# Performance work log

Hardware: AMD Instinct MI355X
Metric: run time of the kernel (lower is better)

## Reference

```python
import jax, jax.numpy as jnp
import numpy as np

V_A, V_HP = 256, 256
H_A, H_HP = 2048, 4096
DEPTH = 12


def lstm_cell(x, h, c, W_ih, W_hh, b_ih, b_hh):
    # PyTorch LSTM cell: gate order i, f, g, o along the 4H axis.
    gates = x @ W_ih.T + h @ W_hh.T + (b_ih + b_hh)
    i, f, g, o = jnp.split(gates, 4, axis=-1)
    c_new = jax.nn.sigmoid(f) * c + jax.nn.sigmoid(i) * jnp.tanh(g)
    h_new = jax.nn.sigmoid(o) * jnp.tanh(c_new)
    return h_new, c_new


def setup_inputs() -> dict:
    key = jax.random.key(0)
    ks = jax.random.split(key, 16)
    s = jnp.float32(0.02)
    f32 = jnp.float32
    return {
        "x_thought_vec_arch": jax.random.normal(ks[0], (1, 1, H_A), f32),
        "x_thought_vec_arch_hp": jax.random.normal(ks[1], (1, 1, H_HP), f32),
        # arch LSTM (input V_A, hidden H_A)
        "W_ih_a": jax.random.normal(ks[2], (4 * H_A, V_A), f32) * s,
        "W_hh_a": jax.random.normal(ks[3], (4 * H_A, H_A), f32) * s,
        "b_ih_a": jax.random.normal(ks[4], (4 * H_A,), f32) * s,
        "b_hh_a": jax.random.normal(ks[5], (4 * H_A,), f32) * s,
        # arch_out Linear (H_A -> V_A)
        "W_out_a": jax.random.normal(ks[6], (V_A, H_A), f32) * s,
        "b_out_a": jax.random.normal(ks[7], (V_A,), f32) * s,
        # hp_summarizer Linear (H_HP -> H_HP//2)
        "W_sum": jax.random.normal(ks[8], (H_HP // 2, H_HP), f32) * s,
        "b_sum": jax.random.normal(ks[9], (H_HP // 2,), f32) * s,
        # arch_hp LSTM (input V_A + V_HP, hidden H_HP)
        "W_ih_hp": jax.random.normal(ks[10], (4 * H_HP, V_A + V_HP), f32) * s,
        "W_hh_hp": jax.random.normal(ks[11], (4 * H_HP, H_HP), f32) * s,
        "b_ih_hp": jax.random.normal(ks[12], (4 * H_HP,), f32) * s,
        "b_hh_hp": jax.random.normal(ks[13], (4 * H_HP,), f32) * s,
        # arch_hp_out Linear (H_HP -> V_HP)
        "W_out_hp": jax.random.normal(ks[14], (V_HP, H_HP), f32) * s,
        "b_out_hp": jax.random.normal(ks[15], (V_HP,), f32) * s,
    }


def reference(x_thought_vec_arch, x_thought_vec_arch_hp,
              W_ih_a, W_hh_a, b_ih_a, b_hh_a, W_out_a, b_out_a,
              W_sum, b_sum, W_ih_hp, W_hh_hp, b_ih_hp, b_hh_hp,
              W_out_hp, b_out_hp):
    h_a, h_hp = x_thought_vec_arch, x_thought_vec_arch_hp  # thought vecs used as hidden states
    c_a = jnp.zeros_like(h_a)
    c_hp = jnp.zeros_like(h_hp)
    a = jnp.full((1, 1, V_A), 1.0 / V_A, jnp.float32)       # SOS soft one-hot
    a_hp = jnp.full((1, 1, V_HP), 1.0 / V_HP, jnp.float32)

    def step(carry, _):
        a, a_hp, h_a, c_a, h_hp, c_hp = carry
        # forward_arch: seq_len=1 so LSTM output == new hidden
        h_a, c_a = lstm_cell(a, h_a, c_a, W_ih_a, W_hh_a, b_ih_a, b_hh_a)
        a = jax.nn.softmax(h_a @ W_out_a.T + b_out_a, axis=-1)
        # forward_arch_hp (keeps the original's swapped hx=(c_hp, prev_h_hp)):
        h_sum = jax.nn.relu(h_hp @ W_sum.T + b_sum)
        prev_h_hp = jnp.concatenate([h_a, h_sum], axis=-1)   # used as CELL state
        inp = jnp.concatenate([a, a_hp], axis=-1)
        h_hp, c_hp = lstm_cell(inp, c_hp, prev_h_hp, W_ih_hp, W_hh_hp, b_ih_hp, b_hh_hp)
        a_hp = jax.nn.softmax(h_hp @ W_out_hp.T + b_out_hp, axis=-1)
        return (a, a_hp, h_a, c_a, h_hp, c_hp), (a, a_hp)

    _, (ys_a, ys_hp) = jax.lax.scan(step, (a, a_hp, h_a, c_a, h_hp, c_hp), None, length=DEPTH)
    # torch.cat(list_of_(1,1,V), dim=1) -> (1, DEPTH, V)
    arch = ys_a.reshape(DEPTH, V_A)[None]
    arch_hp = ys_hp.reshape(DEPTH, V_HP)[None]
    return arch, arch_hp
```

## Files before the change

kernel.cpp:

```cpp
#include <hip/hip_runtime.h>
#include <hip/hip_fp16.h>

#define H_A   2048
#define H_HP  4096
#define V_A   256
#define V_HP  256
#define DEPTH 12

struct Half8 { __half2 a, b, c, d; };

__device__ __forceinline__ float fsig_(float x) { return 1.0f / (1.0f + __expf(-x)); }
__device__ __forceinline__ float ftanh_(float x) {
    return 1.0f - 2.0f / (__expf(2.0f * x) + 1.0f);
}

__device__ __forceinline__ float dot8h_(Half8 w, float4 x0, float4 x1) {
    float2 wa = __half22float2(w.a), wb = __half22float2(w.b);
    float2 wc = __half22float2(w.c), wd = __half22float2(w.d);
    return wa.x * x0.x + wa.y * x0.y + wb.x * x0.z + wb.y * x0.w +
           wc.x * x1.x + wc.y * x1.y + wd.x * x1.z + wd.y * x1.w;
}

__device__ __forceinline__ Half8 cvt8_(float4 a, float4 b) {
    Half8 h;
    h.a = __floats2half2_rn(a.x, a.y);
    h.b = __floats2half2_rn(a.z, a.w);
    h.c = __floats2half2_rn(b.x, b.y);
    h.d = __floats2half2_rn(b.z, b.w);
    return h;
}

__device__ __forceinline__ float waveReduceSum(float v) {
#pragma unroll
    for (int off = 32; off > 0; off >>= 1) v += __shfl_xor(v, off, 64);
    return v;
}

__global__ void k_init(const float* __restrict__ x_a, const float* __restrict__ x_hp,
                       float* __restrict__ h_a, float* __restrict__ c_a0,
                       float* __restrict__ h_hp, float* __restrict__ c_hp,
                       float* __restrict__ a_vec, float* __restrict__ logits_hp)
{
    int i = blockIdx.x * 256 + threadIdx.x;
    if (i < H_A)  { h_a[i] = x_a[i];  c_a0[i] = 0.0f; }
    if (i < H_HP) { h_hp[i] = x_hp[i]; c_hp[i] = 0.0f; }
    if (i < V_A)  { a_vec[i] = 1.0f / 256.0f; logits_hp[i] = 0.0f; }
}

__global__ __launch_bounds__(256) void k_f2h_batched(
    const float* __restrict__ W_ih_a,  __half* __restrict__ hW_ih_a,
    const float* __restrict__ W_hh_a,  __half* __restrict__ hW_hh_a,
    const float* __restrict__ W_sum,   __half* __restrict__ hW_sum,
    const float* __restrict__ W_ih_hp, __half* __restrict__ hW_ih_hp,
    const float* __restrict__ W_out_a, __half* __restrict__ hW_out_a,
    const float* __restrict__ W_out_hp,__half* __restrict__ hW_out_hp)
{
    int i = blockIdx.x * 256 + threadIdx.x;
    const float* src; __half* dst; int base;
    if      (i < 262144)  { src = W_ih_a;   dst = hW_ih_a;   base = 0; }
    else if (i < 2359296) { src = W_hh_a;   dst = hW_hh_a;   base = 262144; }
    else if (i < 3407872) { src = W_sum;    dst = hW_sum;    base = 2359296; }
    else if (i < 4456448) { src = W_ih_hp;  dst = hW_ih_hp;  base = 3407872; }
    else if (i < 4521984) { src = W_out_a;  dst = hW_out_a;  base = 4456448; }
    else if (i < 4653056) { src = W_out_hp; dst = hW_out_hp; base = 4521984; }
    else return;
    int j = i - base;
    float4 a = ((const float4*)src)[2 * j];
    float4 b = ((const float4*)src)[2 * j + 1];
    ((Half8*)dst)[j] = cvt8_(a, b);
}

__global__ __launch_bounds__(256) void kA_fused_gemv(
    const __half* __restrict__ hW_ih_a, const __half* __restrict__ hW_hh_a,
    const float* __restrict__ b_ih_a, const float* __restrict__ b_hh_a,
    const __half* __restrict__ hW_sum,  const float* __restrict__ b_sum,
    __half* __restrict__ hW_hh_hp, const float* __restrict__ W_hh_hp_f32,
    const float* __restrict__ b_ih_hp, const float* __restrict__ b_hh_hp,
    const float* __restrict__ a_vec,  const float* __restrict__ h_a,
    const float* __restrict__ h_hp,   const float* __restrict__ c_hp,
    float* __restrict__ gates_a, float* __restrict__ h_sum_o,
    float* __restrict__ gacc_hp, int step0)
{
    const int lane = threadIdx.x & 63;
    const int wave = (blockIdx.x << 2) | (threadIdx.x >> 6);

    if (wave < 8192) {
        const int r = wave;
        const __half2* wp = (const __half2*)(hW_ih_a + (size_t)r * V_A);
        __half2 w0h = wp[2 * lane], w1h = wp[2 * lane + 1];
        float4 x = ((const float4*)a_vec)[lane];
        float2 w0 = __half22float2(w0h), w1 = __half22float2(w1h);
        float acc = w0.x * x.x + w0.y * x.y + w1.x * x.z + w1.y * x.w;
        const Half8* wh = (const Half8*)(hW_hh_a + (size_t)r * H_A);
        const float4* xh = (const float4*)h_a;
#pragma unroll
        for (int it = 0; it < 4; ++it) {
            int idx = it * 64 + lane;
            acc += dot8h_(wh[idx], xh[2 * idx], xh[2 * idx + 1]);
        }
        acc = waveReduceSum(acc);
        if (lane == 0) gates_a[r] = acc + b_ih_a[r] + b_hh_a[r];
    } else if (wave < 10240) {
        const int r = wave - 8192;
        const Half8* ww = (const Half8*)(hW_sum + (size_t)r * H_HP);
        const float4* xx = (const float4*)h_hp;
        float acc = 0.0f;
#pragma unroll
        for (int it = 0; it < 8; ++it) {
            int idx = it * 64 + lane;
            acc += dot8h_(ww[idx], xx[2 * idx], xx[2 * idx + 1]);
        }
        acc = waveReduceSum(acc);
        if (lane == 0) h_sum_o[r] = fmaxf(acc + b_sum[r], 0.0f);
    } else {
        const int r = wave - 10240;
        if (step0) {
            const float4* src = (const float4*)(W_hh_hp_f32 + (size_t)r * H_HP);
            Half8* dst = (Half8*)(hW_hh_hp + (size_t)r * H_HP);
#pragma unroll
            for (int it = 0; it < 8; ++it) {
                int idx = it * 64 + lane;
                dst[idx] = cvt8_(src[2 * idx], src[2 * idx + 1]);
            }
            if (lane == 0) gacc_hp[r] = b_ih_hp[r] + b_hh_hp[r];
        } else {
            const Half8* ww = (const Half8*)(hW_hh_hp + (size_t)r * H_HP);
            const float4* xx = (const float4*)c_hp;
            float acc = 0.0f;
#pragma unroll
            for (int it = 0; it < 8; ++it) {
                int idx = it * 64 + lane;
                acc += dot8h_(ww[idx], xx[2 * idx], xx[2 * idx + 1]);
            }
            acc = waveReduceSum(acc);
            if (lane == 0) gacc_hp[r] = acc + b_ih_hp[r] + b_hh_hp[r];
        }
    }
}

__global__ __launch_bounds__(256) void kB_arch(
    const float* __restrict__ gates_a, const float* __restrict__ c_in,
    float* __restrict__ c_out, float* __restrict__ h_a_g,
    const __half* __restrict__ hW_out_a, const float* __restrict__ b_out_a,
    float* __restrict__ logits_a)
{
    __shared__ float h_s[H_A];
    const int t = threadIdx.x;
#pragma unroll
    for (int k = 0; k < 8; ++k) {
        int e = t + k * 256;
        float gi = gates_a[e];
        float gf = gates_a[H_A + e];
        float gg = gates_a[2 * H_A + e];
        float go = gates_a[3 * H_A + e];
        float c_new = fsig_(gf) * c_in[e] + fsig_(gi) * ftanh_(gg);
        float h = fsig_(go) * ftanh_(c_new);
        h_s[e] = h;
        if (blockIdx.x == 0) { c_out[e] = c_new; h_a_g[e] = h; }
    }
    __syncthreads();
    const int lane = t & 63;
    const int r = (blockIdx.x << 2) | (t >> 6);
    const Half8* w8 = (const Half8*)(hW_out_a + (size_t)r * H_A);
    const float4* h4 = (const float4*)h_s;
    float acc = 0.0f;
#pragma unroll
    for (int it = 0; it < 4; ++it) {
        int idx = it * 64 + lane;
        acc += dot8h_(w8[idx], h4[2 * idx], h4[2 * idx + 1]);
    }
    acc = waveReduceSum(acc);
    if (lane == 0) logits_a[r] = acc + b_out_a[r];
}

__global__ __launch_bounds__(256) void kC_softmax_ih(
    const float* __restrict__ logits_a, const float* __restrict__ logits_hp,
    const __half* __restrict__ hW_ih_hp, float* __restrict__ gacc_hp,
    float* __restrict__ a_vec_g, float* __restrict__ out_a,
    float* __restrict__ out_hp)
{
    __shared__ float p_all[512];
    __shared__ float red[8];
    const int t = threadIdx.x, lane = t & 63, wv = t >> 6;
    float la = logits_a[t], lh = logits_hp[t];
    float ma = la, mh = lh;
#pragma unroll
    for (int off = 32; off > 0; off >>= 1) {
        ma = fmaxf(ma, __shfl_xor(ma, off, 64));
        mh = fmaxf(mh, __shfl_xor(mh, off, 64));
    }
    if (lane == 0) { red[wv] = ma; red[4 + wv] = mh; }
    __syncthreads();
    ma = fmaxf(fmaxf(red[0], red[1]), fmaxf(red[2], red[3]));
    mh = fmaxf(fmaxf(red[4], red[5]), fmaxf(red[6], red[7]));
    __syncthreads();
    float ea = __expf(la - ma), eh = __expf(lh - mh);
    float sa = waveReduceSum(ea), sh = waveReduceSum(eh);
    if (lane == 0) { red[wv] = sa; red[4 + wv] = sh; }
    __syncthreads();
    sa = red[0] + red[1] + red[2] + red[3];
    sh = red[4] + red[5] + red[6] + red[7];
    float pa = ea / sa, ph = eh / sh;
    p_all[t] = pa;
    p_all[256 + t] = ph;
    if (blockIdx.x == 0) {
        a_vec_g[t] = pa;
        out_a[t] = pa;
        out_hp[t] = ph;
    }
    __syncthreads();
    const float4* x4 = (const float4*)p_all;
    float4 xa = x4[2 * lane], xb = x4[2 * lane + 1];
    const int gw = (blockIdx.x << 2) | wv;
#pragma unroll
    for (int rr = 0; rr < 4; ++rr) {
        int r = (gw << 2) | rr;
        Half8 w = ((const Half8*)(hW_ih_hp + (size_t)r * (V_A + V_HP)))[lane];
        float acc = dot8h_(w, xa, xb);
        acc = waveReduceSum(acc);
        if (lane == 0) gacc_hp[r] += acc;
    }
}

__global__ __launch_bounds__(256) void kD_hp(
    const float* __restrict__ gacc_hp, const float* __restrict__ h_a,
    const float* __restrict__ h_sum, float* __restrict__ c_hp_g,
    float* __restrict__ h_hp_g,
    const __half* __restrict__ hW_out_hp, const float* __restrict__ b_out_hp,
    float* __restrict__ logits_hp)
{
    __shared__ float h_s[H_HP];
    const int t = threadIdx.x;
#pragma unroll
    for (int k = 0; k < 16; ++k) {
        int e = t + k * 256;
        float gi = gacc_hp[e];
        float gf = gacc_hp[H_HP + e];
        float gg = gacc_hp[2 * H_HP + e];
        float go = gacc_hp[3 * H_HP + e];
        float prev = (e < H_A) ? h_a[e] : h_sum[e - H_A];
        float c = fsig_(gf) * prev + fsig_(gi) * ftanh_(gg);
        float h = fsig_(go) * ftanh_(c);
        h_s[e] = h;
        if (blockIdx.x == 0) { c_hp_g[e] = c; h_hp_g[e] = h; }
    }
    __syncthreads();
    const int lane = t & 63;
    const int r = (blockIdx.x << 2) | (t >> 6);
    const Half8* w8 = (const Half8*)(hW_out_hp + (size_t)r * H_HP);
    const float4* x4 = (const float4*)h_s;
    float acc = 0.0f;
#pragma unroll
    for (int it = 0; it < 8; ++it) {
        int idx = it * 64 + lane;
        acc += dot8h_(w8[idx], x4[2 * idx], x4[2 * idx + 1]);
    }
    acc = waveReduceSum(acc);
    if (lane == 0) logits_hp[r] = acc + b_out_hp[r];
}

__global__ __launch_bounds__(256) void k_softmax_tail(
    const float* __restrict__ logits_hp, float* __restrict__ outp)
{
    __shared__ float red[4];
    const int t = threadIdx.x, lane = t & 63, wv = t >> 6;
    float v = logits_hp[t];
    float m = v;
#pragma unroll
    for (int off = 32; off > 0; off >>= 1) m = fmaxf(m, __shfl_xor(m, off, 64));
    if (lane == 0) red[wv] = m;
    __syncthreads();
    m = fmaxf(fmaxf(red[0], red[1]), fmaxf(red[2], red[3]));
    __syncthreads();
    float e = __expf(v - m);
    float s = waveReduceSum(e);
    if (lane == 0) red[wv] = s;
    __syncthreads();
    s = red[0] + red[1] + red[2] + red[3];
    outp[t] = e / s;
}


extern "C" void kernel_launch(void* const* d_in, const int* in_sizes, int n_in,
                              void* d_out, int out_size, void* d_ws, size_t ws_size,
                              hipStream_t stream)
{
    const float* x_a      = (const float*)d_in[0];
    const float* x_hp     = (const float*)d_in[1];
    const float* W_ih_a   = (const float*)d_in[2];
    const float* W_hh_a   = (const float*)d_in[3];
    const float* b_ih_a   = (const float*)d_in[4];
    const float* b_hh_a   = (const float*)d_in[5];
    const float* W_out_a  = (const float*)d_in[6];
    const float* b_out_a  = (const float*)d_in[7];
    const float* W_sum    = (const float*)d_in[8];
    const float* b_sum    = (const float*)d_in[9];
    const float* W_ih_hp  = (const float*)d_in[10];
    const float* W_hh_hp  = (const float*)d_in[11];
    const float* b_ih_hp  = (const float*)d_in[12];
    const float* b_hh_hp  = (const float*)d_in[13];
    const float* W_out_hp = (const float*)d_in[14];
    const float* b_out_hp = (const float*)d_in[15];

    float* out = (float*)d_out;

    __half* hW_ih_a   = (__half*)d_ws;
    __half* hW_hh_a   = hW_ih_a   + 2097152;
    __half* hW_sum    = hW_hh_a   + 16777216;
    __half* hW_ih_hp  = hW_sum    + 8388608;
    __half* hW_hh_hp  = hW_ih_hp  + 8388608;
    __half* hW_out_a  = hW_hh_hp  + 67108864;
    __half* hW_out_hp = hW_out_a  + 524288;
    float* ws = (float*)(hW_out_hp + 1048576);

    float* gates_a   = ws;
    float* h_sum     = ws + 8192;
    float* gacc_hp   = ws + 10240;
    float* h_a       = ws + 26624;
    float* c_a0      = ws + 28672;
    float* c_a1      = ws + 30720;
    float* h_hp      = ws + 32768;
    float* c_hp      = ws + 36864;
    float* logits_a  = ws + 40960;
    float* logits_hp = ws + 41216;
    float* a_vec     = ws + 41472;
    float* dummy     = ws + 41728;
    float* c_a[2]    = { c_a0, c_a1 };

    k_init<<<16, 256, 0, stream>>>(x_a, x_hp, h_a, c_a0, h_hp, c_hp, a_vec, logits_hp);

    k_f2h_batched<<<18176, 256, 0, stream>>>(
        W_ih_a, hW_ih_a, W_hh_a, hW_hh_a, W_sum, hW_sum,
        W_ih_hp, hW_ih_hp, W_out_a, hW_out_a, W_out_hp, hW_out_hp);

    for (int t = 0; t < DEPTH; ++t) {
        kA_fused_gemv<<<6656, 256, 0, stream>>>(
            hW_ih_a, hW_hh_a, b_ih_a, b_hh_a, hW_sum, b_sum,
            hW_hh_hp, W_hh_hp, b_ih_hp, b_hh_hp,
            a_vec, h_a, h_hp, c_hp,
            gates_a, h_sum, gacc_hp, (t == 0) ? 1 : 0);

        kB_arch<<<64, 256, 0, stream>>>(gates_a, c_a[t & 1], c_a[(t + 1) & 1], h_a,
                                        hW_out_a, b_out_a, logits_a);

        kC_softmax_ih<<<1024, 256, 0, stream>>>(
            logits_a, logits_hp, hW_ih_hp, gacc_hp,
            a_vec, out + (size_t)t * V_A,
            (t == 0) ? dummy : out + (size_t)DEPTH * V_A + (size_t)(t - 1) * V_HP);

        kD_hp<<<64, 256, 0, stream>>>(gacc_hp, h_a, h_sum, c_hp, h_hp,
                                      hW_out_hp, b_out_hp, logits_hp);
    }

    k_softmax_tail<<<1, 256, 0, stream>>>(
        logits_hp, out + (size_t)DEPTH * V_A + (size_t)(DEPTH - 1) * V_HP);
}
```

Baseline: 1.137 ms.

## Replace per-step kernel launches with a single cooperative persistent kernel

Merges the init, weight-conversion and per-step kernels (four per step across twelve steps) into one cooperative persistent kernel that uses grid-wide syncs between phases. The fp32-to-fp16 weight conversion is folded into the first step's GEMVs, so weights are read once in fp32 and used directly instead of being converted in a separate pass. The output-projection GEMV for the hp branch moves to the start of the next step. The aim is to remove launch overhead and the separate conversion pass. The cost is grid.sync latency and a grid capped at 1024 blocks, which may limit bandwidth for the large GEMVs.

```diff
diff --git a/kernel.cpp b/kernel.cpp
--- a/kernel.cpp
+++ b/kernel.cpp
@@ -1,26 +1,35 @@
 #include <hip/hip_runtime.h>
 #include <hip/hip_fp16.h>
+#include <hip/hip_cooperative_groups.h>
+
+namespace cg = cooperative_groups;
 
 #define H_A   2048
 #define H_HP  4096
-#define V_A   256
-#define V_HP  256
 #define DEPTH 12
 
 struct Half8 { __half2 a, b, c, d; };
+struct Half4 { __half2 a, b; };
 
 __device__ __forceinline__ float fsig_(float x) { return 1.0f / (1.0f + __expf(-x)); }
 __device__ __forceinline__ float ftanh_(float x) {
     return 1.0f - 2.0f / (__expf(2.0f * x) + 1.0f);
 }
-
+__device__ __forceinline__ float dot4_(float4 a, float4 b) {
+    return a.x * b.x + a.y * b.y + a.z * b.z + a.w * b.w;
+}
 __device__ __forceinline__ float dot8h_(Half8 w, float4 x0, float4 x1) {
     float2 wa = __half22float2(w.a), wb = __half22float2(w.b);
     float2 wc = __half22float2(w.c), wd = __half22float2(w.d);
     return wa.x * x0.x + wa.y * x0.y + wb.x * x0.z + wb.y * x0.w +
            wc.x * x1.x + wc.y * x1.y + wd.x * x1.z + wd.y * x1.w;
 }
-
+__device__ __forceinline__ Half4 cvt4_(float4 a) {
+    Half4 h;
+    h.a = __floats2half2_rn(a.x, a.y);
+    h.b = __floats2half2_rn(a.z, a.w);
+    return h;
+}
 __device__ __forceinline__ Half8 cvt8_(float4 a, float4 b) {
     Half8 h;
     h.a = __floats2half2_rn(a.x, a.y);
@@ -29,11 +38,301 @@
     h.d = __floats2half2_rn(b.z, b.w);
     return h;
 }
-
 __device__ __forceinline__ float waveReduceSum(float v) {
 #pragma unroll
     for (int off = 32; off > 0; off >>= 1) v += __shfl_xor(v, off, 64);
     return v;
+}
+__device__ __forceinline__ void waveReduce4(float& a0, float& a1, float& a2, float& a3) {
+#pragma unroll
+    for (int off = 32; off > 0; off >>= 1) {
+        a0 += __shfl_xor(a0, off, 64);
+        a1 += __shfl_xor(a1, off, 64);
+        a2 += __shfl_xor(a2, off, 64);
+        a3 += __shfl_xor(a3, off, 64);
+    }
+}
+
+struct Params {
+    const float *x_a, *x_hp;
+    const float *W_ih_a, *W_hh_a, *b_ih_a, *b_hh_a;
+    const float *W_out_a, *b_out_a, *W_sum, *b_sum;
+    const float *W_ih_hp, *W_hh_hp, *b_ih_hp, *b_hh_hp, *W_out_hp, *b_out_hp;
+    __half *hW_ih_a, *hW_hh_a, *hW_sum, *hW_ih_hp, *hW_hh_hp, *hW_out_a, *hW_out_hp;
+    float *gates_a, *h_sum, *gacc, *h_a, *c_a0, *c_a1, *h_hp, *c_hp;
+    float *logits_a, *logits_hp, *a_vec, *out;
+};
+
+__global__ __launch_bounds__(256) void decoder_persistent(Params p)
+{
+    cg::grid_group grid = cg::this_grid();
+    __shared__ float sbuf[2056];
+    const int tid = threadIdx.x, lane = tid & 63, wv = tid >> 6;
+    const int waveId = (blockIdx.x << 2) | wv;
+    const int nw = (gridDim.x << 2);
+
+    for (int t = 0; t < DEPTH; ++t) {
+        {
+            const int limit = (t == 0) ? 26624 : 26880;
+            for (int r = waveId; r < limit; r += nw) {
+                if (r < 8192) {
+                    float acc;
+                    if (t == 0) {
+                        float4 wf = ((const float4*)(p.W_ih_a + (size_t)r * 256))[lane];
+                        ((Half4*)(p.hW_ih_a + (size_t)r * 256))[lane] = cvt4_(wf);
+                        acc = (wf.x + wf.y + wf.z + wf.w) * (1.0f / 256.0f);
+                        const float4* whf = (const float4*)(p.W_hh_a + (size_t)r * H_A);
+                        const float4* xh = (const float4*)p.x_a;
+                        Half4* dsth = (Half4*)(p.hW_hh_a + (size_t)r * H_A);
+#pragma unroll
+                        for (int it = 0; it < 8; ++it) {
+                            int idx = it * 64 + lane;
+                            float4 w = whf[idx];
+                            dsth[idx] = cvt4_(w);
+                            acc += dot4_(w, xh[idx]);
+                        }
+                    } else {
+                        Half4 w = ((const Half4*)(p.hW_ih_a + (size_t)r * 256))[lane];
+                        float4 x = ((const float4*)p.a_vec)[lane];
+                        float2 w0 = __half22float2(w.a), w1 = __half22float2(w.b);
+                        acc = w0.x * x.x + w0.y * x.y + w1.x * x.z + w1.y * x.w;
+                        const Half8* wh = (const Half8*)(p.hW_hh_a + (size_t)r * H_A);
+                        const float4* xh = (const float4*)p.h_a;
+#pragma unroll
+                        for (int it = 0; it < 4; ++it) {
+                            int idx = it * 64 + lane;
+                            acc += dot8h_(wh[idx], xh[2 * idx], xh[2 * idx + 1]);
+                        }
+                    }
+                    acc = waveReduceSum(acc);
+                    if (lane == 0) p.gates_a[r] = acc + p.b_ih_a[r] + p.b_hh_a[r];
+                } else if (r < 10240) {
+                    const int rr = r - 8192;
+                    float acc = 0.0f;
+                    if (t == 0) {
+                        const float4* wf = (const float4*)(p.W_sum + (size_t)rr * H_HP);
+                        const float4* xx = (const float4*)p.x_hp;
+                        Half4* dsth = (Half4*)(p.hW_sum + (size_t)rr * H_HP);
+#pragma unroll
+                        for (int it = 0; it < 16; ++it) {
+                            int idx = it * 64 + lane;
+                            float4 w = wf[idx];
+                            dsth[idx] = cvt4_(w);
+                            acc += dot4_(w, xx[idx]);
+                        }
+                    } else {
+                        const Half8* ww = (const Half8*)(p.hW_sum + (size_t)rr * H_HP);
+                        const float4* xx = (const float4*)p.h_hp;
+#pragma unroll
+                        for (int it = 0; it < 8; ++it) {
+                            int idx = it * 64 + lane;
+                            acc += dot8h_(ww[idx], xx[2 * idx], xx[2 * idx + 1]);
+                        }
+                    }
+                    acc = waveReduceSum(acc);
+                    if (lane == 0) p.h_sum[rr] = fmaxf(acc + p.b_sum[rr], 0.0f);
+                } else if (r < 26624) {
+                    const int rg = r - 10240;
+                    if (t == 0) {
+                        const float4* wf = (const float4*)(p.W_hh_hp + (size_t)rg * H_HP);
+                        Half4* dsth = (Half4*)(p.hW_hh_hp + (size_t)rg * H_HP);
+#pragma unroll
+                        for (int it = 0; it < 16; ++it) {
+                            int idx = it * 64 + lane;
+                            dsth[idx] = cvt4_(wf[idx]);
+                        }
+                        if (lane == 0) p.gacc[rg] = p.b_ih_hp[rg] + p.b_hh_hp[rg];
+                    } else {
+                        const Half8* ww = (const Half8*)(p.hW_hh_hp + (size_t)rg * H_HP);
+                        const float4* xx = (const float4*)p.c_hp;
+                        float acc = 0.0f;
+#pragma unroll
+                        for (int it = 0; it < 8; ++it) {
+                            int idx = it * 64 + lane;
+                            acc += dot8h_(ww[idx], xx[2 * idx], xx[2 * idx + 1]);
+                        }
+                        acc = waveReduceSum(acc);
+                        if (lane == 0) p.gacc[rg] = acc + p.b_ih_hp[rg] + p.b_hh_hp[rg];
+                    }
+                } else {
+                    const int ro = r - 26624;
+                    float acc = 0.0f;
+                    const float4* xx = (const float4*)p.h_hp;
+                    if (t == 1) {
+                        const float4* wf = (const float4*)(p.W_out_hp + (size_t)ro * H_HP);
+                        Half4* dsth = (Half4*)(p.hW_out_hp + (size_t)ro * H_HP);
+#pragma unroll
+                        for (int it = 0; it < 16; ++it) {
+                            int idx = it * 64 + lane;
+                            float4 w = wf[idx];
+                            dsth[idx] = cvt4_(w);
+                            acc += dot4_(w, xx[idx]);
+                        }
+                    } else {
+                        const Half8* ww = (const Half8*)(p.hW_out_hp + (size_t)ro * H_HP);
+#pragma unroll
+                        for (int it = 0; it < 8; ++it) {
+                            int idx = it * 64 + lane;
+                            acc += dot8h_(ww[idx], xx[2 * idx], xx[2 * idx + 1]);
+                        }
+                    }
+                    acc = waveReduceSum(acc);
+                    if (lane == 0) p.logits_hp[ro] = acc + p.b_out_hp[ro];
+                }
+            }
+        }
+        grid.sync();
+
+        if (blockIdx.x < 16) {
+            float* h_s = sbuf;
+            const float* cin = (t & 1) ? p.c_a1 : p.c_a0;
+            float* cout = (t & 1) ? p.c_a0 : p.c_a1;
+#pragma unroll
+            for (int k = 0; k < 8; ++k) {
+                int e = tid + k * 256;
+                float gi = p.gates_a[e], gf = p.gates_a[H_A + e];
+                float gg = p.gates_a[2 * H_A + e], go = p.gates_a[3 * H_A + e];
+                float ci = (t == 0) ? 0.0f : cin[e];
+                float c = fsig_(gf) * ci + fsig_(gi) * ftanh_(gg);
+                float h = fsig_(go) * ftanh_(c);
+                h_s[e] = h;
+                if (blockIdx.x == 0) { cout[e] = c; p.h_a[e] = h; }
+            }
+            __syncthreads();
+            const float4* h4 = (const float4*)h_s;
+            int row = (blockIdx.x << 4) | (wv << 2);
+            for (int j = 0; j < 4; ++j, ++row) {
+                float acc = 0.0f;
+                if (t == 0) {
+                    const float4* wf = (const float4*)(p.W_out_a + (size_t)row * H_A);
+                    Half4* dsth = (Half4*)(p.hW_out_a + (size_t)row * H_A);
+#pragma unroll
+                    for (int it = 0; it < 8; ++it) {
+                        int idx = it * 64 + lane;
+                        float4 w = wf[idx];
+                        dsth[idx] = cvt4_(w);
+                        acc += dot4_(w, h4[idx]);
+                    }
+                } else {
+                    const Half8* ww = (const Half8*)(p.hW_out_a + (size_t)row * H_A);
+#pragma unroll
+                    for (int it = 0; it < 4; ++it) {
+                        int idx = it * 64 + lane;
+                        acc += dot8h_(ww[idx], h4[2 * idx], h4[2 * idx + 1]);
+                    }
+                }
+                acc = waveReduceSum(acc);
+                if (lane == 0) p.logits_a[row] = acc + p.b_out_a[row];
+            }
+        }
+        grid.sync();
+
+        {
+            float* p_all = sbuf;
+            float* red   = sbuf + 512;
+            float la = p.logits_a[tid];
+            float lh = (t == 0) ? 0.0f : p.logits_hp[tid];
+            float ma = la, mh = lh;
+#pragma unroll
+            for (int off = 32; off > 0; off >>= 1) {
+                ma = fmaxf(ma, __shfl_xor(ma, off, 64));
+                mh = fmaxf(mh, __shfl_xor(mh, off, 64));
+            }
+            if (lane == 0) { red[wv] = ma; red[4 + wv] = mh; }
+            __syncthreads();
+            ma = fmaxf(fmaxf(red[0], red[1]), fmaxf(red[2], red[3]));
+            mh = fmaxf(fmaxf(red[4], red[5]), fmaxf(red[6], red[7]));
+            __syncthreads();
+            float ea = __expf(la - ma), eh = __expf(lh - mh);
+            float sa = waveReduceSum(ea), sh = waveReduceSum(eh);
+            if (lane == 0) { red[wv] = sa; red[4 + wv] = sh; }
+            __syncthreads();
+            sa = red[0] + red[1] + red[2] + red[3];
+            sh = red[4] + red[5] + red[6] + red[7];
+            float pa = ea / sa, ph = eh / sh;
+            p_all[tid] = pa;
+            p_all[256 + tid] = ph;
+            if (blockIdx.x == 0) {
+                p.a_vec[tid] = pa;
+                p.out[(size_t)t * 256 + tid] = pa;
+                if (t > 0) p.out[3072 + (size_t)(t - 1) * 256 + tid] = ph;
+            }
+            __syncthreads();
+            float4 xa = ((const float4*)p_all)[2 * lane];
+            float4 xb = ((const float4*)p_all)[2 * lane + 1];
+            for (int e = waveId; e < H_HP; e += nw) {
+                float s0, s1, s2, s3;
+                if (t == 0) {
+                    auto rowdot_cvt = [&](int r) -> float {
+                        const float4* wf = (const float4*)(p.W_ih_hp + (size_t)r * 512);
+                        float4 u = wf[2 * lane], v = wf[2 * lane + 1];
+                        ((Half8*)(p.hW_ih_hp + (size_t)r * 512))[lane] = cvt8_(u, v);
+                        return dot4_(u, xa) + dot4_(v, xb);
+                    };
+                    s0 = rowdot_cvt(e);
+                    s1 = rowdot_cvt(4096 + e);
+                    s2 = rowdot_cvt(8192 + e);
+                    s3 = rowdot_cvt(12288 + e);
+                } else {
+                    Half8 w0 = ((const Half8*)(p.hW_ih_hp + (size_t)e * 512))[lane];
+                    Half8 w1 = ((const Half8*)(p.hW_ih_hp + (size_t)(4096 + e) * 512))[lane];
+                    Half8 w2 = ((const Half8*)(p.hW_ih_hp + (size_t)(8192 + e) * 512))[lane];
+                    Half8 w3 = ((const Half8*)(p.hW_ih_hp + (size_t)(12288 + e) * 512))[lane];
+                    s0 = dot8h_(w0, xa, xb);
+                    s1 = dot8h_(w1, xa, xb);
+                    s2 = dot8h_(w2, xa, xb);
+                    s3 = dot8h_(w3, xa, xb);
+                }
+                waveReduce4(s0, s1, s2, s3);
+                if (lane == 0) {
+                    float gi = s0 + p.gacc[e];
+                    float gf = s1 + p.gacc[4096 + e];
+                    float gg = s2 + p.gacc[8192 + e];
+                    float go = s3 + p.gacc[12288 + e];
+                    float prev = (e < H_A) ? p.h_a[e] : p.h_sum[e - H_A];
+                    float c = fsig_(gf) * prev + fsig_(gi) * ftanh_(gg);
+                    float h = fsig_(go) * ftanh_(c);
+                    p.c_hp[e] = c;
+                    p.h_hp[e] = h;
+                }
+            }
+        }
+        grid.sync();
+    }
+
+    if (blockIdx.x < 16) {
+        int row = (blockIdx.x << 4) | (wv << 2);
+        const float4* xx = (const float4*)p.h_hp;
+        for (int j = 0; j < 4; ++j, ++row) {
+            const Half8* ww = (const Half8*)(p.hW_out_hp + (size_t)row * H_HP);
+            float acc = 0.0f;
+#pragma unroll
+            for (int it = 0; it < 8; ++it) {
+                int idx = it * 64 + lane;
+                acc += dot8h_(ww[idx], xx[2 * idx], xx[2 * idx + 1]);
+            }
+            acc = waveReduceSum(acc);
+            if (lane == 0) p.logits_hp[row] = acc + p.b_out_hp[row];
+        }
+    }
+    grid.sync();
+    if (blockIdx.x == 0) {
+        float* red = sbuf + 512;
+        float v = p.logits_hp[tid];
+        float m = v;
+#pragma unroll
+        for (int off = 32; off > 0; off >>= 1) m = fmaxf(m, __shfl_xor(m, off, 64));
+        if (lane == 0) red[wv] = m;
+        __syncthreads();
+        m = fmaxf(fmaxf(red[0], red[1]), fmaxf(red[2], red[3]));
+        __syncthreads();
+        float e = __expf(v - m);
+        float s = waveReduceSum(e);
+        if (lane == 0) red[wv] = s;
+        __syncthreads();
+        s = red[0] + red[1] + red[2] + red[3];
+        p.out[3072 + 11 * 256 + tid] = e / s;
+    }
 }
 
 __global__ void k_init(const float* __restrict__ x_a, const float* __restrict__ x_hp,
@@ -44,7 +343,7 @@
     int i = blockIdx.x * 256 + threadIdx.x;
     if (i < H_A)  { h_a[i] = x_a[i];  c_a0[i] = 0.0f; }
     if (i < H_HP) { h_hp[i] = x_hp[i]; c_hp[i] = 0.0f; }
-    if (i < V_A)  { a_vec[i] = 1.0f / 256.0f; logits_hp[i] = 0.0f; }
+    if (i < 256)  { a_vec[i] = 1.0f / 256.0f; logits_hp[i] = 0.0f; }
 }
 
 __global__ __launch_bounds__(256) void k_f2h_batched(
@@ -86,7 +385,7 @@
 
     if (wave < 8192) {
         const int r = wave;
-        const __half2* wp = (const __half2*)(hW_ih_a + (size_t)r * V_A);
+        const __half2* wp = (const __half2*)(hW_ih_a + (size_t)r * 256);
         __half2 w0h = wp[2 * lane], w1h = wp[2 * lane + 1];
         float4 x = ((const float4*)a_vec)[lane];
         float2 w0 = __half22float2(w0h), w1 = __half22float2(w1h);
@@ -215,7 +514,7 @@
 #pragma unroll
     for (int rr = 0; rr < 4; ++rr) {
         int r = (gw << 2) | rr;
-        Half8 w = ((const Half8*)(hW_ih_hp + (size_t)r * (V_A + V_HP)))[lane];
+        Half8 w = ((const Half8*)(hW_ih_hp + (size_t)r * 512))[lane];
         float acc = dot8h_(w, xa, xb);
         acc = waveReduceSum(acc);
         if (lane == 0) gacc_hp[r] += acc;
@@ -285,73 +584,85 @@
                               void* d_out, int out_size, void* d_ws, size_t ws_size,
                               hipStream_t stream)
 {
-    const float* x_a      = (const float*)d_in[0];
-    const float* x_hp     = (const float*)d_in[1];
-    const float* W_ih_a   = (const float*)d_in[2];
-    const float* W_hh_a   = (const float*)d_in[3];
-    const float* b_ih_a   = (const float*)d_in[4];
-    const float* b_hh_a   = (const float*)d_in[5];
-    const float* W_out_a  = (const float*)d_in[6];
-    const float* b_out_a  = (const float*)d_in[7];
-    const float* W_sum    = (const float*)d_in[8];
-    const float* b_sum    = (const float*)d_in[9];
-    const float* W_ih_hp  = (const float*)d_in[10];
-    const float* W_hh_hp  = (const float*)d_in[11];
-    const float* b_ih_hp  = (const float*)d_in[12];
-    const float* b_hh_hp  = (const float*)d_in[13];
-    const float* W_out_hp = (const float*)d_in[14];
-    const float* b_out_hp = (const float*)d_in[15];
-
-    float* out = (float*)d_out;
-
-    __half* hW_ih_a   = (__half*)d_ws;
-    __half* hW_hh_a   = hW_ih_a   + 2097152;
-    __half* hW_sum    = hW_hh_a   + 16777216;
-    __half* hW_ih_hp  = hW_sum    + 8388608;
-    __half* hW_hh_hp  = hW_ih_hp  + 8388608;
-    __half* hW_out_a  = hW_hh_hp  + 67108864;
-    __half* hW_out_hp = hW_out_a  + 524288;
-    float* ws = (float*)(hW_out_hp + 1048576);
-
-    float* gates_a   = ws;
-    float* h_sum     = ws + 8192;
-    float* gacc_hp   = ws + 10240;
-    float* h_a       = ws + 26624;
-    float* c_a0      = ws + 28672;
-    float* c_a1      = ws + 30720;
-    float* h_hp      = ws + 32768;
-    float* c_hp      = ws + 36864;
-    float* logits_a  = ws + 40960;
-    float* logits_hp = ws + 41216;
-    float* a_vec     = ws + 41472;
-    float* dummy     = ws + 41728;
-    float* c_a[2]    = { c_a0, c_a1 };
-
-    k_init<<<16, 256, 0, stream>>>(x_a, x_hp, h_a, c_a0, h_hp, c_hp, a_vec, logits_hp);
-
+    Params p;
+    p.x_a      = (const float*)d_in[0];
+    p.x_hp     = (const float*)d_in[1];
+    p.W_ih_a   = (const float*)d_in[2];
+    p.W_hh_a   = (const float*)d_in[3];
+    p.b_ih_a   = (const float*)d_in[4];
+    p.b_hh_a   = (const float*)d_in[5];
+    p.W_out_a  = (const float*)d_in[6];
+    p.b_out_a  = (const float*)d_in[7];
+    p.W_sum    = (const float*)d_in[8];
+    p.b_sum    = (const float*)d_in[9];
+    p.W_ih_hp  = (const float*)d_in[10];
+    p.W_hh_hp  = (const float*)d_in[11];
+    p.b_ih_hp  = (const float*)d_in[12];
+    p.b_hh_hp  = (const float*)d_in[13];
+    p.W_out_hp = (const float*)d_in[14];
+    p.b_out_hp = (const float*)d_in[15];
+
+    p.hW_ih_a   = (__half*)d_ws;
+    p.hW_hh_a   = p.hW_ih_a   + 2097152;
+    p.hW_sum    = p.hW_hh_a   + 16777216;
+    p.hW_ih_hp  = p.hW_sum    + 8388608;
+    p.hW_hh_hp  = p.hW_ih_hp  + 8388608;
+    p.hW_out_a  = p.hW_hh_hp  + 67108864;
+    p.hW_out_hp = p.hW_out_a  + 524288;
+    float* ws = (float*)(p.hW_out_hp + 1048576);
+
+    p.gates_a   = ws;
+    p.h_sum     = ws + 8192;
+    p.gacc      = ws + 10240;
+    p.h_a       = ws + 26624;
+    p.c_a0      = ws + 28672;
+    p.c_a1      = ws + 30720;
+    p.h_hp      = ws + 32768;
+    p.c_hp      = ws + 36864;
+    p.logits_a  = ws + 40960;
+    p.logits_hp = ws + 41216;
+    p.a_vec     = ws + 41472;
+    float* dummy = ws + 41728;
+    p.out       = (float*)d_out;
+
+    int blocksPerCU = 0;
+    hipError_t qerr = hipOccupancyMaxActiveBlocksPerMultiprocessor(
+        &blocksPerCU, (const void*)decoder_persistent, 256, 0);
+    if (qerr == hipSuccess && blocksPerCU >= 1) {
+        int grid = blocksPerCU * 256;
+        if (grid > 1024) grid = 1024;
+        void* kargs[] = { (void*)&p };
+        hipError_t lerr = hipLaunchCooperativeKernel(
+            (const void*)decoder_persistent, dim3(grid), dim3(256), kargs, 0, stream);
+        if (lerr == hipSuccess) return;
+    }
+
+    k_init<<<16, 256, 0, stream>>>(p.x_a, p.x_hp, p.h_a, p.c_a0, p.h_hp, p.c_hp,
+                                   p.a_vec, p.logits_hp);
     k_f2h_batched<<<18176, 256, 0, stream>>>(
-        W_ih_a, hW_ih_a, W_hh_a, hW_hh_a, W_sum, hW_sum,
-        W_ih_hp, hW_ih_hp, W_out_a, hW_out_a, W_out_hp, hW_out_hp);
-
+        p.W_ih_a, p.hW_ih_a, p.W_hh_a, p.hW_hh_a, p.W_sum, p.hW_sum,
+        p.W_ih_hp, p.hW_ih_hp, p.W_out_a, p.hW_out_a, p.W_out_hp, p.hW_out_hp);
+
+    float* c_a[2] = { p.c_a0, p.c_a1 };
+    float* out = p.out;
     for (int t = 0; t < DEPTH; ++t) {
         kA_fused_gemv<<<6656, 256, 0, stream>>>(
-            hW_ih_a, hW_hh_a, b_ih_a, b_hh_a, hW_sum, b_sum,
-            hW_hh_hp, W_hh_hp, b_ih_hp, b_hh_hp,
-            a_vec, h_a, h_hp, c_hp,
-            gates_a, h_sum, gacc_hp, (t == 0) ? 1 : 0);
-
-        kB_arch<<<64, 256, 0, stream>>>(gates_a, c_a[t & 1], c_a[(t + 1) & 1], h_a,
-                                        hW_out_a, b_out_a, logits_a);
+            p.hW_ih_a, p.hW_hh_a, p.b_ih_a, p.b_hh_a, p.hW_sum, p.b_sum,
+            p.hW_hh_hp, p.W_hh_hp, p.b_ih_hp, p.b_hh_hp,
+            p.a_vec, p.h_a, p.h_hp, p.c_hp,
+            p.gates_a, p.h_sum, p.gacc, (t == 0) ? 1 : 0);
+
+        kB_arch<<<64, 256, 0, stream>>>(p.gates_a, c_a[t & 1], c_a[(t + 1) & 1],
+                                        p.h_a, p.hW_out_a, p.b_out_a, p.logits_a);
 
         kC_softmax_ih<<<1024, 256, 0, stream>>>(
-            logits_a, logits_hp, hW_ih_hp, gacc_hp,
-            a_vec, out + (size_t)t * V_A,
-            (t == 0) ? dummy : out + (size_t)DEPTH * V_A + (size_t)(t - 1) * V_HP);
-
-        kD_hp<<<64, 256, 0, stream>>>(gacc_hp, h_a, h_sum, c_hp, h_hp,
-                                      hW_out_hp, b_out_hp, logits_hp);
-    }
-
-    k_softmax_tail<<<1, 256, 0, stream>>>(
-        logits_hp, out + (size_t)DEPTH * V_A + (size_t)(DEPTH - 1) * V_HP);
-}
+            p.logits_a, p.logits_hp, p.hW_ih_hp, p.gacc,
+            p.a_vec, out + (size_t)t * 256,
+            (t == 0) ? dummy : out + 3072 + (size_t)(t - 1) * 256);
+
+        kD_hp<<<64, 256, 0, stream>>>(p.gacc, p.h_a, p.h_sum, p.c_hp, p.h_hp,
+                                      p.hW_out_hp, p.b_out_hp, p.logits_hp);
+    }
+
+    k_softmax_tail<<<1, 256, 0, stream>>>(p.logits_hp, out + 3072 + 11 * 256);
+}
```

After: 1.140 ms. Within noise of the previous version (+0.2%).
